# Performance work log

Measured on AMD Instinct MI355X. Metric: run time of the kernel, lower is better.

Reference implementation:

```python
import jax, jax.numpy as jnp
import numpy as np

N_NODES = 100000
N_GRAPHS = 64

def gcn_conv(x, edge_index, W, b, num_nodes):
    # PyG GCNConv: x' = D^-1/2 (A + I) D^-1/2 (x W) + b
    h = x @ W  # [N, out]
    row, col = edge_index[0], edge_index[1]
    loops = jnp.arange(num_nodes, dtype=row.dtype)
    src = jnp.concatenate([row, loops])  # message source (x_j)
    dst = jnp.concatenate([col, loops])  # aggregation target
    deg = jax.ops.segment_sum(jnp.ones_like(src, dtype=h.dtype), dst,
                              num_segments=num_nodes)
    dinv = jnp.where(deg > 0, jax.lax.rsqrt(deg), 0.0)
    norm = dinv[src] * dinv[dst]  # [E+N]
    msgs = h[src] * norm[:, None]  # gather-transform
    out = jax.ops.segment_sum(msgs, dst, num_segments=num_nodes)  # scatter
    return out + b

def global_mean_pool(x, batch, num_graphs):
    sums = jax.ops.segment_sum(x, batch, num_segments=num_graphs)
    cnts = jax.ops.segment_sum(jnp.ones((x.shape[0],), x.dtype), batch,
                               num_segments=num_graphs)
    return sums / jnp.maximum(cnts, 1.0)[:, None]

def setup_inputs() -> dict:
    key = jax.random.key(0)
    ks = jax.random.split(key, 12)
    d_in, d_hid, d_mid, d_out = 128, 128, 20, 10
    n_edges = 1600000
    x = jax.random.normal(ks[0], (N_NODES, d_in), dtype=jnp.float32)
    edge_index = jax.random.randint(ks[1], (2, n_edges), 0, N_NODES, dtype=jnp.int64)
    batch = jnp.sort(jax.random.randint(ks[2], (N_NODES,), 0, N_GRAPHS, dtype=jnp.int64))
    def glorot(k, fan_in, fan_out):
        s = (6.0 / (fan_in + fan_out)) ** 0.5
        return jax.random.uniform(k, (fan_in, fan_out), jnp.float32, -s, s)
    return {
        "x": x, "edge_index": edge_index, "batch": batch,
        "W1": glorot(ks[3], d_in, d_hid), "b1": jnp.zeros((d_hid,), jnp.float32),
        "W2": glorot(ks[4], d_hid, d_hid), "b2": jnp.zeros((d_hid,), jnp.float32),
        "fc1_W": glorot(ks[5], d_hid, d_mid), "fc1_b": jnp.zeros((d_mid,), jnp.float32),
        "fc2_W": glorot(ks[6], d_mid, d_out), "fc2_b": jnp.zeros((d_out,), jnp.float32),
    }

def reference(x, edge_index, batch, W1, b1, W2, b2, fc1_W, fc1_b, fc2_W, fc2_b):
    # eval mode: dropout is identity
    h = gcn_conv(x, edge_index, W1, b1, N_NODES)
    h = jax.nn.elu(h)
    h = gcn_conv(h, edge_index, W2, b2, N_NODES)
    g = global_mean_pool(h, batch, N_GRAPHS)  # [G, hidden]
    g = jax.nn.relu(g @ fc1_W + fc1_b)
    g = g @ fc2_W + fc2_b
    return jax.nn.log_softmax(g, axis=1)
```

## Files before the change

### kernel.cpp

```cpp
#include <hip/hip_runtime.h>
#include <math.h>

#define DH 128
#define BCAP 16384

typedef __bf16 bf8_t __attribute__((ext_vector_type(8)));
typedef short short8 __attribute__((ext_vector_type(8)));
typedef float f4_t __attribute__((ext_vector_type(4)));
typedef float f2_t __attribute__((ext_vector_type(2)));

__device__ inline unsigned short f2b(float f) {
    unsigned int u = __builtin_bit_cast(unsigned int, f);
    u = u + 0x7fffu + ((u >> 16) & 1u);
    return (unsigned short)(u >> 16);
}
__device__ inline float b2f(unsigned short h) {
    return __builtin_bit_cast(float, (unsigned int)h << 16);
}

__global__ __launch_bounds__(256) void k_bucket(const int* __restrict__ row,
                                                const int* __restrict__ col,
                                                int E, int nbuck, int chunk,
                                                unsigned int* __restrict__ pairs,
                                                int* __restrict__ bcur) {
    __shared__ int lcnt[256];
    __shared__ int lbase[256];
    __shared__ unsigned int srec[8192];
    int t = threadIdx.x;
    int e0 = blockIdx.x * chunk;
    int e1 = min(e0 + chunk, E);
    lcnt[t] = 0;
    __syncthreads();
    for (int i = e0 + t; i < e1; i += 256) {
        int d = col[i];
        int b = d >> 9;
        int slot = atomicAdd(&lcnt[b], 1);
        srec[i - e0] = ((unsigned int)b << 22) | ((unsigned int)(d & 511) << 13)
                     | (unsigned int)slot;
    }
    __syncthreads();
    if (t < nbuck) {
        int c = lcnt[t];
        lbase[t] = (c > 0) ? atomicAdd(&bcur[t * 16], c) : 0;
    }
    __syncthreads();
    for (int i = e0 + t; i < e1; i += 256) {
        unsigned int r = srec[i - e0];
        int b = r >> 22;
        unsigned int dl = (r >> 13) & 511u;
        int slot = (int)(r & 8191u);
        int g = lbase[b] + slot;
        if (g < BCAP)
            pairs[(size_t)b * BCAP + g] = ((unsigned int)row[i] << 9) | dl;
    }
}

__global__ __launch_bounds__(256) void k_build(const unsigned int* __restrict__ pairs,
                                               const int* __restrict__ bcur,
                                               int nbuck, int N,
                                               int* __restrict__ off,
                                               int* __restrict__ dpd,
                                               float* __restrict__ dinv,
                                               int* __restrict__ csr) {
    __shared__ int cnt2[512];
    __shared__ int pd2[512];
    __shared__ int excl[512];
    __shared__ int curi[512];
    __shared__ int stmp[256];
    int b = blockIdx.x, t = threadIdx.x;
    int cnt = min(bcur[b * 16], BCAP);
    int base = b * BCAP;
    int node0 = b << 9;
    int nodes = min(512, N - node0);
    cnt2[t] = 0; cnt2[t + 256] = 0;
    __syncthreads();
    const unsigned int* pp = pairs + (size_t)b * BCAP;
    for (int i = t; i < cnt; i += 256)
        atomicAdd(&cnt2[pp[i] & 511u], 1);
    __syncthreads();
    pd2[t] = (cnt2[t] + 15) & ~15;
    pd2[t + 256] = (cnt2[t + 256] + 15) & ~15;
    __syncthreads();
    stmp[t] = pd2[2 * t] + pd2[2 * t + 1];
    __syncthreads();
    for (int d = 1; d < 256; d <<= 1) {
        int v = (t >= d) ? stmp[t - d] : 0;
        __syncthreads();
        stmp[t] += v;
        __syncthreads();
    }
    int pre = (t == 0) ? 0 : stmp[t - 1];
    excl[2 * t] = pre;
    excl[2 * t + 1] = pre + pd2[2 * t];
    __syncthreads();
    if (t < nodes) {
        off[node0 + t] = base + excl[t];
        dpd[node0 + t] = pd2[t];
        dinv[node0 + t] = rsqrtf((float)(cnt2[t] + 1));
    }
    int t2 = t + 256;
    if (t2 < nodes) {
        off[node0 + t2] = base + excl[t2];
        dpd[node0 + t2] = pd2[t2];
        dinv[node0 + t2] = rsqrtf((float)(cnt2[t2] + 1));
    }
    curi[t] = excl[t]; curi[t + 256] = excl[t + 256];
    __syncthreads();
    for (int i = t; i < cnt; i += 256) {
        unsigned int p = pp[i];
        int d = (int)(p & 511u);
        int slot = atomicAdd(&curi[d], 1);
        if (slot < BCAP) csr[base + slot] = (int)(p >> 9);
    }
    for (int n = t; n < 512; n += 256) {
        int e0 = excl[n] + cnt2[n];
        int e1 = min(excl[n] + pd2[n], BCAP);
        for (int k = e0; k < e1; k++) csr[base + k] = N;
    }
}

__global__ void k_prepW(const float* __restrict__ W1, const float* __restrict__ W2,
                        unsigned short* __restrict__ Wt1, unsigned short* __restrict__ Wt2) {
    int t = blockIdx.x * blockDim.x + threadIdx.x;
    int v = t & 16383;
    int k = v >> 7, n = v & 127;
    if (t < 16384) {
        Wt1[n * DH + k] = f2b(W1[k * DH + n]);
    } else {
        int p = ((k & 15) << 3) | (k >> 4);
        Wt2[n * DH + p] = f2b(W2[k * DH + n]);
    }
}

__global__ __launch_bounds__(256) void k_gemm_mfma(const void* __restrict__ Xin, int x_is_bf16,
                                                   const unsigned short* __restrict__ Wt,
                                                   const float* __restrict__ dinv,
                                                   unsigned char* __restrict__ Y, int nrows) {
    __shared__ unsigned short Xs[64 * 136];
    __shared__ unsigned short Ws[128 * 136];
    int t = threadIdx.x;
    int row0 = blockIdx.x * 64;

    for (int v = t; v < 128 * 32; v += 256) {
        int n = v >> 5, kq = v & 31;
        ushort4 w = ((const ushort4*)Wt)[v];
        *(ushort4*)&Ws[n * 136 + kq * 4] = w;
    }
    if (x_is_bf16) {
        const unsigned short* X = (const unsigned short*)Xin;
        for (int v = t; v < 64 * 32; v += 256) {
            int r = v >> 5, cq = v & 31;
            int gr = row0 + r;
            ushort4 h;
            if (gr < nrows) h = ((const ushort4*)X)[(size_t)gr * 32 + cq];
            else { h.x = 0; h.y = 0; h.z = 0; h.w = 0; }
            *(ushort4*)&Xs[r * 136 + cq * 4] = h;
        }
    } else {
        const float* X = (const float*)Xin;
        for (int v = t; v < 64 * 32; v += 256) {
            int r = v >> 5, cq = v & 31;
            int gr = row0 + r;
            ushort4 h;
            if (gr < nrows) {
                float4 xv = ((const float4*)X)[(size_t)gr * 32 + cq];
                h.x = f2b(xv.x); h.y = f2b(xv.y); h.z = f2b(xv.z); h.w = f2b(xv.w);
            } else { h.x = 0; h.y = 0; h.z = 0; h.w = 0; }
            *(ushort4*)&Xs[r * 136 + cq * 4] = h;
        }
    }
    __syncthreads();

    int w = t >> 6;
    int lane = t & 63;
    int quad = lane >> 4;
    int l16 = lane & 15;
    int rw = w * 16;

    f4_t acc[8];
#pragma unroll
    for (int j = 0; j < 8; j++) acc[j] = (f4_t){0.f, 0.f, 0.f, 0.f};

#pragma unroll
    for (int kk = 0; kk < 4; kk++) {
        int k0 = kk * 32;
        bf8_t a = __builtin_bit_cast(bf8_t,
            *(const short8*)&Xs[(rw + l16) * 136 + k0 + quad * 8]);
#pragma unroll
        for (int j = 0; j < 8; j++) {
            bf8_t b = __builtin_bit_cast(bf8_t,
                *(const short8*)&Ws[(j * 16 + l16) * 136 + k0 + quad * 8]);
            acc[j] = __builtin_amdgcn_mfma_f32_16x16x32_bf16(a, b, acc[j], 0, 0, 0);
        }
    }

#pragma unroll
    for (int reg = 0; reg < 4; reg++) {
        int r = row0 + rw + quad * 4 + reg;
        if (r < nrows) {
            float dv = dinv[r];
            float v0 = acc[0][reg] * dv, v1 = acc[1][reg] * dv;
            float v2 = acc[2][reg] * dv, v3 = acc[3][reg] * dv;
            float v4 = acc[4][reg] * dv, v5 = acc[5][reg] * dv;
            float v6 = acc[6][reg] * dv, v7 = acc[7][reg] * dv;
            int d0 = __builtin_amdgcn_cvt_pk_fp8_f32(v0, v1, 0, false);
            d0 = __builtin_amdgcn_cvt_pk_fp8_f32(v2, v3, d0, true);
            int d1 = __builtin_amdgcn_cvt_pk_fp8_f32(v4, v5, 0, false);
            d1 = __builtin_amdgcn_cvt_pk_fp8_f32(v6, v7, d1, true);
            *(uint2*)&Y[(size_t)r * DH + l16 * 8] = make_uint2((unsigned)d0, (unsigned)d1);
        }
    }
}

#define AGG_ROUND(IDX)                                                     \
    {                                                                      \
        int ea = be + 2 * i;                                               \
        int j0 = IDX(ea);      int j1 = IDX(ea + 2);                       \
        int j2 = IDX(ea + 4);  int j3 = IDX(ea + 6);                       \
        int j4 = IDX(ea + 8);  int j5 = IDX(ea + 10);                      \
        int j6 = IDX(ea + 12); int j7 = IDX(ea + 14);                      \
        unsigned int u0 = Tw[(j0 << 5) + l5];                              \
        unsigned int u1 = Tw[(j1 << 5) + l5];                              \
        unsigned int u2 = Tw[(j2 << 5) + l5];                              \
        unsigned int u3 = Tw[(j3 << 5) + l5];                              \
        unsigned int u4 = Tw[(j4 << 5) + l5];                              \
        unsigned int u5 = Tw[(j5 << 5) + l5];                              \
        unsigned int u6 = Tw[(j6 << 5) + l5];                              \
        unsigned int u7 = Tw[(j7 << 5) + l5];                              \
        accA01 += __builtin_amdgcn_cvt_pk_f32_fp8(u0, false);              \
        accA23 += __builtin_amdgcn_cvt_pk_f32_fp8(u0, true);               \
        accB01 += __builtin_amdgcn_cvt_pk_f32_fp8(u1, false);              \
        accB23 += __builtin_amdgcn_cvt_pk_f32_fp8(u1, true);               \
        accA01 += __builtin_amdgcn_cvt_pk_f32_fp8(u2, false);              \
        accA23 += __builtin_amdgcn_cvt_pk_f32_fp8(u2, true);               \
        accB01 += __builtin_amdgcn_cvt_pk_f32_fp8(u3, false);              \
        accB23 += __builtin_amdgcn_cvt_pk_f32_fp8(u3, true);               \
        accA01 += __builtin_amdgcn_cvt_pk_f32_fp8(u4, false);              \
        accA23 += __builtin_amdgcn_cvt_pk_f32_fp8(u4, true);               \
        accB01 += __builtin_amdgcn_cvt_pk_f32_fp8(u5, false);              \
        accB23 += __builtin_amdgcn_cvt_pk_f32_fp8(u5, true);               \
        accA01 += __builtin_amdgcn_cvt_pk_f32_fp8(u6, false);              \
        accA23 += __builtin_amdgcn_cvt_pk_f32_fp8(u6, true);               \
        accB01 += __builtin_amdgcn_cvt_pk_f32_fp8(u7, false);              \
        accB23 += __builtin_amdgcn_cvt_pk_f32_fp8(u7, true);               \
    }

__global__ __launch_bounds__(256) void k_agg(const unsigned char* __restrict__ T,
                                             unsigned short* __restrict__ Out,
                                             const float* __restrict__ dinv,
                                             const int* __restrict__ off,
                                             const int* __restrict__ dpd,
                                             const int* __restrict__ csr,
                                             const float* __restrict__ bias,
                                             int elu, int N) {
    __shared__ int ofs[4];
    __shared__ int dps[4];
    __shared__ float dv4[4];
    __shared__ int sidx[320];
    int t = threadIdx.x;
    int d0 = blockIdx.x * 4;
    if (t < 4) {
        int n = min(d0 + t, N - 1);
        ofs[t] = off[n];
        dps[t] = dpd[n];
        dv4[t] = dinv[n];
    }
    __syncthreads();
    int s0 = ofs[0];
    int span = ofs[3] + dps[3] - s0;
    int scnt = min(span, 320);
    for (int k = t; k < scnt; k += 256) sidx[k] = csr[s0 + k];
    __syncthreads();

    int w = t >> 6;
    int lane = t & 63;
    int half = lane >> 5;
    int l5 = lane & 31;
    const unsigned int* Tw = (const unsigned int*)T;

    int nd = d0 + w;
    if (nd < N) {
        int eL = ofs[w] - s0;
        int pdw = dps[w];
        int K = pdw >> 1;

        f2_t accA01, accA23;
        f2_t accB01 = (f2_t){0.f, 0.f}, accB23 = (f2_t){0.f, 0.f};
        {
            unsigned int u = Tw[(nd << 5) + l5];
            if (half) u = 0;
            accA01 = __builtin_amdgcn_cvt_pk_f32_fp8(u, false);
            accA23 = __builtin_amdgcn_cvt_pk_f32_fp8(u, true);
        }

        int be = eL + half;
        if (eL + pdw <= scnt) {
#define IDX_L(e) sidx[e]
            for (int i = 0; i < K; i += 8) AGG_ROUND(IDX_L)
#undef IDX_L
        } else {
            const int* gp = csr + s0;
#define IDX_G(e) gp[e]
            for (int i = 0; i < K; i += 8) AGG_ROUND(IDX_G)
#undef IDX_G
        }

        float a0 = accA01[0] + accB01[0];
        float a1 = accA01[1] + accB01[1];
        float a2 = accA23[0] + accB23[0];
        float a3 = accA23[1] + accB23[1];
        a0 += __shfl_xor(a0, 32);
        a1 += __shfl_xor(a1, 32);
        a2 += __shfl_xor(a2, 32);
        a3 += __shfl_xor(a3, 32);

        if (!half) {
            int c0 = ((l5 & 1) << 6) | (l5 >> 1);
            float dv = dv4[w];
            float o0 = a0 * dv + bias[c0];
            float o1 = a1 * dv + bias[c0 + 16];
            float o2 = a2 * dv + bias[c0 + 32];
            float o3 = a3 * dv + bias[c0 + 48];
            if (elu) {
                o0 = o0 > 0.f ? o0 : __expf(o0) - 1.f;
                o1 = o1 > 0.f ? o1 : __expf(o1) - 1.f;
                o2 = o2 > 0.f ? o2 : __expf(o2) - 1.f;
                o3 = o3 > 0.f ? o3 : __expf(o3) - 1.f;
            }
            unsigned int p0 = (unsigned int)f2b(o0) | ((unsigned int)f2b(o1) << 16);
            unsigned int p1 = (unsigned int)f2b(o2) | ((unsigned int)f2b(o3) << 16);
            *(uint2*)&Out[(size_t)nd * DH + (l5 << 2)] = make_uint2(p0, p1);
        }
    }
}

__global__ __launch_bounds__(256) void k_pool(const unsigned int* __restrict__ H32,
                                              const int* __restrict__ batch,
                                              float* __restrict__ Gsum,
                                              int* __restrict__ cnts, int N) {
    int g = blockIdx.x;
    int p = blockIdx.y;
    int t = threadIdx.x;
    int lane = t & 63;
    int rg = t >> 6;
    int lo = 0, hi = N;
    while (lo < hi) { int m = (lo + hi) >> 1; if (batch[m] < g) lo = m + 1; else hi = m; }
    int s = lo;
    hi = N;
    while (lo < hi) { int m = (lo + hi) >> 1; if (batch[m] < g + 1) lo = m + 1; else hi = m; }
    int e = lo;
    int len = e - s;
    int parts = (int)gridDim.y;
    int chunk = (len + parts - 1) / parts;
    int i0 = s + p * chunk;
    int i1 = min(i0 + chunk, e);
    float a0 = 0.f, a1 = 0.f;
    for (int i = i0 + rg; i < i1; i += 4) {
        unsigned int v = H32[(size_t)i * 64 + lane];
        a0 += b2f((unsigned short)(v & 0xffffu));
        a1 += b2f((unsigned short)(v >> 16));
    }
    __shared__ float ps[4][DH];
    ps[rg][lane * 2] = a0;
    ps[rg][lane * 2 + 1] = a1;
    __syncthreads();
    if (t < DH) {
        float v = ps[0][t] + ps[1][t] + ps[2][t] + ps[3][t];
        atomicAdd(&Gsum[g * DH + t], v);
    }
    if (p == 0 && t == 0) cnts[g] = len;
}

__global__ __launch_bounds__(64) void k_head(const float* __restrict__ Gsum,
                                             const int* __restrict__ cnts,
                                             const float* __restrict__ W1,
                                             const float* __restrict__ b1,
                                             const float* __restrict__ W2,
                                             const float* __restrict__ b2,
                                             float* __restrict__ out) {
    int g = blockIdx.x;
    int t = threadIdx.x;
    __shared__ float gv[DH];
    __shared__ float mid[20];
    __shared__ float o[10];
    float inv = 1.f / fmaxf((float)cnts[g], 1.f);
    for (int i = t; i < DH; i += 64) {
        int c = ((i & 7) << 4) | (i >> 3);
        gv[c] = Gsum[g * DH + i] * inv;
    }
    __syncthreads();
    if (t < 20) {
        float a = b1[t];
        for (int k = 0; k < DH; k++) a += gv[k] * W1[k * 20 + t];
        mid[t] = fmaxf(a, 0.f);
    }
    __syncthreads();
    if (t < 10) {
        float a = b2[t];
        for (int k = 0; k < 20; k++) a += mid[k] * W2[k * 10 + t];
        o[t] = a;
    }
    __syncthreads();
    if (t == 0) {
        float m = -1e30f;
        for (int j = 0; j < 10; j++) m = fmaxf(m, o[j]);
        float ssum = 0.f;
        for (int j = 0; j < 10; j++) ssum += expf(o[j] - m);
        float l = logf(ssum);
        for (int j = 0; j < 10; j++) out[g * 10 + j] = o[j] - m - l;
    }
}

extern "C" void kernel_launch(void* const* d_in, const int* in_sizes, int n_in,
                              void* d_out, int out_size, void* d_ws, size_t ws_size,
                              hipStream_t stream) {
    const float* x    = (const float*)d_in[0];
    const int*   ei   = (const int*)d_in[1];
    const int*   batch= (const int*)d_in[2];
    const float* W1   = (const float*)d_in[3];
    const float* b1   = (const float*)d_in[4];
    const float* W2   = (const float*)d_in[5];
    const float* b2   = (const float*)d_in[6];
    const float* fc1W = (const float*)d_in[7];
    const float* fc1b = (const float*)d_in[8];
    const float* fc2W = (const float*)d_in[9];
    const float* fc2b = (const float*)d_in[10];
    float* out = (float*)d_out;

    int N = in_sizes[0] / DH;
    int E = in_sizes[1] / 2;
    int G = out_size / 10;
    int nbuck = (N + 511) >> 9;

    char* p = (char*)d_ws;
    auto alloc = [&](size_t bytes) {
        char* r = p;
        p += (bytes + 255) & ~(size_t)255;
        return r;
    };
    size_t pairs_bytes = (size_t)nbuck * BCAP * 4;
    size_t t8_bytes = (size_t)(N + 1) * DH;
    char* region = alloc(pairs_bytes > t8_bytes ? pairs_bytes : t8_bytes);
    unsigned int*   pairs = (unsigned int*)region;
    unsigned char*  t8    = (unsigned char*)region;
    unsigned short* a1 = (unsigned short*)alloc((size_t)N * DH * 2);
    int*   csr  = (int*)alloc((size_t)nbuck * BCAP * 4);
    int*   off  = (int*)alloc((size_t)N * 4);
    int*   dpd  = (int*)alloc((size_t)N * 4);
    float* dinv = (float*)alloc((size_t)N * 4);
    unsigned short* Wt1 = (unsigned short*)alloc(DH * DH * 2);
    unsigned short* Wt2 = (unsigned short*)alloc(DH * DH * 2);
    float* Gsum = (float*)alloc((size_t)G * DH * 4);
    int*   bcur = (int*)alloc(256 * 16 * 4);
    int*   cnts = (int*)alloc((size_t)G * 4);

    const int* row = ei;
    const int* col = ei + E;

    (void)hipMemsetAsync(Gsum, 0, (size_t)G * DH * 4 + 256 * 16 * 4, stream);

    const int chunk = 8192;
    int ablocks = (E + chunk - 1) / chunk;
    k_bucket<<<ablocks, 256, 0, stream>>>(row, col, E, nbuck, chunk, pairs, bcur);
    k_build<<<nbuck, 256, 0, stream>>>(pairs, bcur, nbuck, N, off, dpd, dinv, csr);
    (void)hipMemsetAsync(t8 + (size_t)N * DH, 0, DH, stream);
    k_prepW<<<128, 256, 0, stream>>>(W1, W2, Wt1, Wt2);

    int gblocks = (N + 63) / 64;
    int mblocks = (N + 3) / 4;
    k_gemm_mfma<<<gblocks, 256, 0, stream>>>(x, 0, Wt1, dinv, t8, N);
    k_agg<<<mblocks, 256, 0, stream>>>(t8, a1, dinv, off, dpd, csr, b1, 1, N);
    k_gemm_mfma<<<gblocks, 256, 0, stream>>>(a1, 1, Wt2, dinv, t8, N);
    k_agg<<<mblocks, 256, 0, stream>>>(t8, a1, dinv, off, dpd, csr, b2, 0, N);

    dim3 pg(G, 32);
    k_pool<<<pg, 256, 0, stream>>>((const unsigned int*)a1, batch, Gsum, cnts, N);
    k_head<<<G, 64, 0, stream>>>(Gsum, cnts, fc1W, fc1b, fc2W, fc2b, out);
}
```

Baseline: 317.6 us.

## Fold self-loops into CSR and process 16 nodes per aggregation block

The CSR build now inserts each node's self-loop as the first entry of its padded adjacency list and counts it in the degree, so the aggregation no longer needs a separate self-term load. Each aggregation block now handles 16 nodes (4 per wave) with a larger shared index cache, and each half-wave takes a contiguous half of the edge list instead of interleaving even and odd edges. Bias loads are hoisted out of the per-node loop and gather addresses are computed as byte offsets. The wider blocks cut launch count and amortize index staging, but padded lists can grow by one entry and per-wave work becomes serial across four nodes.

```diff
diff --git a/kernel.cpp b/kernel.cpp
--- a/kernel.cpp
+++ b/kernel.cpp
@@ -72,7 +72,8 @@
     int base = b * BCAP;
     int node0 = b << 9;
     int nodes = min(512, N - node0);
-    cnt2[t] = 0; cnt2[t + 256] = 0;
+    cnt2[t] = (t < nodes) ? 1 : 0;
+    cnt2[t + 256] = (t + 256 < nodes) ? 1 : 0;
     __syncthreads();
     const unsigned int* pp = pairs + (size_t)b * BCAP;
     for (int i = t; i < cnt; i += 256)
@@ -93,19 +94,28 @@
     excl[2 * t] = pre;
     excl[2 * t + 1] = pre + pd2[2 * t];
     __syncthreads();
+    for (int n = t; n < 512; n += 256) {
+        int avail = BCAP - excl[n];
+        int pdc = pd2[n];
+        if (pdc > avail) pdc = (avail > 0) ? (avail & ~15) : 0;
+        pd2[n] = pdc;
+    }
+    __syncthreads();
     if (t < nodes) {
         off[node0 + t] = base + excl[t];
         dpd[node0 + t] = pd2[t];
-        dinv[node0 + t] = rsqrtf((float)(cnt2[t] + 1));
+        dinv[node0 + t] = rsqrtf((float)cnt2[t]);
     }
     int t2 = t + 256;
     if (t2 < nodes) {
         off[node0 + t2] = base + excl[t2];
         dpd[node0 + t2] = pd2[t2];
-        dinv[node0 + t2] = rsqrtf((float)(cnt2[t2] + 1));
-    }
-    curi[t] = excl[t]; curi[t + 256] = excl[t + 256];
-    __syncthreads();
+        dinv[node0 + t2] = rsqrtf((float)cnt2[t2]);
+    }
+    curi[t] = excl[t] + 1; curi[t + 256] = excl[t + 256] + 1;
+    __syncthreads();
+    for (int n = t; n < nodes; n += 256)
+        if (excl[n] < BCAP) csr[base + excl[n]] = node0 + n;
     for (int i = t; i < cnt; i += 256) {
         unsigned int p = pp[i];
         int d = (int)(p & 511u);
@@ -114,7 +124,7 @@
     }
     for (int n = t; n < 512; n += 256) {
         int e0 = excl[n] + cnt2[n];
-        int e1 = min(excl[n] + pd2[n], BCAP);
+        int e1 = excl[n] + pd2[n];
         for (int k = e0; k < e1; k++) csr[base + k] = N;
     }
 }
@@ -214,19 +224,23 @@
 
 #define AGG_ROUND(IDX)                                                     \
     {                                                                      \
-        int ea = be + 2 * i;                                               \
-        int j0 = IDX(ea);      int j1 = IDX(ea + 2);                       \
-        int j2 = IDX(ea + 4);  int j3 = IDX(ea + 6);                       \
-        int j4 = IDX(ea + 8);  int j5 = IDX(ea + 10);                      \
-        int j6 = IDX(ea + 12); int j7 = IDX(ea + 14);                      \
-        unsigned int u0 = Tw[(j0 << 5) + l5];                              \
-        unsigned int u1 = Tw[(j1 << 5) + l5];                              \
-        unsigned int u2 = Tw[(j2 << 5) + l5];                              \
-        unsigned int u3 = Tw[(j3 << 5) + l5];                              \
-        unsigned int u4 = Tw[(j4 << 5) + l5];                              \
-        unsigned int u5 = Tw[(j5 << 5) + l5];                              \
-        unsigned int u6 = Tw[(j6 << 5) + l5];                              \
-        unsigned int u7 = Tw[(j7 << 5) + l5];                              \
+        int ea = be + i;                                                   \
+        unsigned v0 = ((unsigned)IDX(ea)     << 7) | l5b;                  \
+        unsigned v1 = ((unsigned)IDX(ea + 1) << 7) | l5b;                  \
+        unsigned v2 = ((unsigned)IDX(ea + 2) << 7) | l5b;                  \
+        unsigned v3 = ((unsigned)IDX(ea + 3) << 7) | l5b;                  \
+        unsigned v4 = ((unsigned)IDX(ea + 4) << 7) | l5b;                  \
+        unsigned v5 = ((unsigned)IDX(ea + 5) << 7) | l5b;                  \
+        unsigned v6 = ((unsigned)IDX(ea + 6) << 7) | l5b;                  \
+        unsigned v7 = ((unsigned)IDX(ea + 7) << 7) | l5b;                  \
+        unsigned int u0 = *(const unsigned int*)(Tb + v0);                 \
+        unsigned int u1 = *(const unsigned int*)(Tb + v1);                 \
+        unsigned int u2 = *(const unsigned int*)(Tb + v2);                 \
+        unsigned int u3 = *(const unsigned int*)(Tb + v3);                 \
+        unsigned int u4 = *(const unsigned int*)(Tb + v4);                 \
+        unsigned int u5 = *(const unsigned int*)(Tb + v5);                 \
+        unsigned int u6 = *(const unsigned int*)(Tb + v6);                 \
+        unsigned int u7 = *(const unsigned int*)(Tb + v7);                 \
         accA01 += __builtin_amdgcn_cvt_pk_f32_fp8(u0, false);              \
         accA23 += __builtin_amdgcn_cvt_pk_f32_fp8(u0, true);               \
         accB01 += __builtin_amdgcn_cvt_pk_f32_fp8(u1, false);              \
@@ -253,22 +267,22 @@
                                              const int* __restrict__ csr,
                                              const float* __restrict__ bias,
                                              int elu, int N) {
-    __shared__ int ofs[4];
-    __shared__ int dps[4];
-    __shared__ float dv4[4];
-    __shared__ int sidx[320];
+    __shared__ int ofs[16];
+    __shared__ int pds[16];
+    __shared__ float dv16[16];
+    __shared__ int sidx[768];
     int t = threadIdx.x;
-    int d0 = blockIdx.x * 4;
-    if (t < 4) {
+    int d0 = blockIdx.x * 16;
+    if (t < 16) {
         int n = min(d0 + t, N - 1);
         ofs[t] = off[n];
-        dps[t] = dpd[n];
-        dv4[t] = dinv[n];
+        pds[t] = dpd[n];
+        dv16[t] = dinv[n];
     }
     __syncthreads();
     int s0 = ofs[0];
-    int span = ofs[3] + dps[3] - s0;
-    int scnt = min(span, 320);
+    int span = ofs[15] + pds[15] - s0;
+    int scnt = min(span, 768);
     for (int k = t; k < scnt; k += 256) sidx[k] = csr[s0 + k];
     __syncthreads();
 
@@ -276,25 +290,25 @@
     int lane = t & 63;
     int half = lane >> 5;
     int l5 = lane & 31;
-    const unsigned int* Tw = (const unsigned int*)T;
-
-    int nd = d0 + w;
-    if (nd < N) {
-        int eL = ofs[w] - s0;
-        int pdw = dps[w];
-        int K = pdw >> 1;
-
-        f2_t accA01, accA23;
+    unsigned l5b = (unsigned)(l5 << 2);
+    const char* Tb = (const char*)T;
+
+    int c0 = ((l5 & 1) << 6) | (l5 >> 1);
+    float bb0 = bias[c0], bb1 = bias[c0 + 16], bb2 = bias[c0 + 32], bb3 = bias[c0 + 48];
+
+    for (int ni = 0; ni < 4; ni++) {
+        int nl = 4 * w + ni;
+        int nd = d0 + nl;
+        if (nd >= N) break;
+        int eL = ofs[nl] - s0;
+        int pd = pds[nl];
+        int K = pd >> 1;
+        int be = eL + half * K;
+
+        f2_t accA01 = (f2_t){0.f, 0.f}, accA23 = (f2_t){0.f, 0.f};
         f2_t accB01 = (f2_t){0.f, 0.f}, accB23 = (f2_t){0.f, 0.f};
-        {
-            unsigned int u = Tw[(nd << 5) + l5];
-            if (half) u = 0;
-            accA01 = __builtin_amdgcn_cvt_pk_f32_fp8(u, false);
-            accA23 = __builtin_amdgcn_cvt_pk_f32_fp8(u, true);
-        }
-
-        int be = eL + half;
-        if (eL + pdw <= scnt) {
+
+        if (eL + pd <= scnt) {
 #define IDX_L(e) sidx[e]
             for (int i = 0; i < K; i += 8) AGG_ROUND(IDX_L)
 #undef IDX_L
@@ -315,12 +329,11 @@
         a3 += __shfl_xor(a3, 32);
 
         if (!half) {
-            int c0 = ((l5 & 1) << 6) | (l5 >> 1);
-            float dv = dv4[w];
-            float o0 = a0 * dv + bias[c0];
-            float o1 = a1 * dv + bias[c0 + 16];
-            float o2 = a2 * dv + bias[c0 + 32];
-            float o3 = a3 * dv + bias[c0 + 48];
+            float dv = dv16[nl];
+            float o0 = a0 * dv + bb0;
+            float o1 = a1 * dv + bb1;
+            float o2 = a2 * dv + bb2;
+            float o3 = a3 * dv + bb3;
             if (elu) {
                 o0 = o0 > 0.f ? o0 : __expf(o0) - 1.f;
                 o1 = o1 > 0.f ? o1 : __expf(o1) - 1.f;
@@ -467,7 +480,7 @@
     k_prepW<<<128, 256, 0, stream>>>(W1, W2, Wt1, Wt2);
 
     int gblocks = (N + 63) / 64;
-    int mblocks = (N + 3) / 4;
+    int mblocks = (N + 15) / 16;
     k_gemm_mfma<<<gblocks, 256, 0, stream>>>(x, 0, Wt1, dinv, t8, N);
     k_agg<<<mblocks, 256, 0, stream>>>(t8, a1, dinv, off, dpd, csr, b1, 1, N);
     k_gemm_mfma<<<gblocks, 256, 0, stream>>>(a1, 1, Wt2, dinv, t8, N);
```

After: 298.4 us. 6.0% less time.
